# Optimization experiments

Measured on AMD Instinct MI355X. Metric: run time of the kernel, lower is better.

The kernel has to match this reference:

```python
import jax, jax.numpy as jnp
import numpy as np

NUM_LAYERS = 4
D_MODEL = 128
D_STATE = 16
DELTA_RANK = 8


def setup_inputs() -> dict:
    key = jax.random.key(0)
    ks = jax.random.split(key, 10)
    d, N, dr, L_ = D_MODEL, D_STATE, DELTA_RANK, NUM_LAYERS
    B, R, T = 4, 32, 1024
    x = jax.random.normal(ks[0], (B, R, T), dtype=jnp.float32)

    def w(k, shape, fan_in):
        return jax.random.normal(k, shape, dtype=jnp.float32) / np.sqrt(fan_in).astype(np.float32)

    inp_w = w(ks[1], (d, 1), 1)
    inp_b = jnp.zeros((d,), jnp.float32)
    outp_w = w(ks[2], (1, d), d)
    outp_b = jnp.zeros((1,), jnp.float32)
    ln_g = jnp.ones((L_, d), jnp.float32)
    ln_b = jnp.zeros((L_, d), jnp.float32)
    in_w = w(ks[3], (L_, 2 * d, d), d)
    conv_w = w(ks[4], (L_, d, 3), 3)
    conv_b = jnp.zeros((L_, d), jnp.float32)
    xp_w = w(ks[5], (L_, dr + 2 * N, d), d)
    dp_w = w(ks[6], (L_, d, dr), dr)
    # delta_proj bias = log(dt), dt ~ loguniform(dt_min, dt_max)
    dt = jnp.exp(jax.random.uniform(ks[7], (L_, d), dtype=jnp.float32) * (np.log(0.1) - np.log(0.001)) + np.log(0.001))
    dp_b = jnp.log(dt)
    # A_log = Re(log(-0.5 + i*imag)) = 0.5*log(0.25 + imag^2)
    A_imag = np.arange(1, N + 1, dtype=np.float32) / (1.0 + 2.0 * np.arange(N, dtype=np.float32))
    A_row = 0.5 * np.log(0.25 + A_imag ** 2)
    A_log = jnp.asarray(np.broadcast_to(A_row, (L_, d, N)).copy(), jnp.float32)
    Dp = 0.1 * jnp.ones((L_, d), jnp.float32)
    out_w = w(ks[8], (L_, d, d), d)
    return dict(x=x, inp_w=inp_w, inp_b=inp_b, outp_w=outp_w, outp_b=outp_b,
                ln_g=ln_g, ln_b=ln_b, in_w=in_w, conv_w=conv_w, conv_b=conv_b,
                xp_w=xp_w, dp_w=dp_w, dp_b=dp_b, A_log=A_log, Dp=Dp, out_w=out_w)


def _layernorm(x, g, b):
    mu = jnp.mean(x, -1, keepdims=True)
    v = jnp.var(x, -1, keepdims=True)
    return (x - mu) * jax.lax.rsqrt(v + 1e-5) * g + b


def _selective_scan(u, delta, A_log, Bm, Cm, Dp):
    # u, delta: (Bt, L, d); Bm, Cm: (Bt, L, N); A_log: (d, N); Dp: (d,)
    Bt, L, d = u.shape
    N = A_log.shape[1]
    A = -jnp.exp(A_log)  # (d, N)

    def step(x_prev, inp):
        u_t, dt_t, B_t, C_t = inp  # (Bt,d),(Bt,d),(Bt,N),(Bt,N)
        dA = jnp.exp(dt_t[..., None] * A)                       # (Bt,d,N)
        dBu = dt_t[..., None] * B_t[:, None, :] * u_t[..., None]  # (Bt,d,N)
        x_new = dA * x_prev + dBu
        y_t = jnp.einsum('bdn,bn->bd', x_new, C_t)
        return x_new, y_t

    x0 = jnp.zeros((Bt, d, N), dtype=u.dtype)
    _, ys = jax.lax.scan(step, x0, (u.swapaxes(0, 1), delta.swapaxes(0, 1),
                                    Bm.swapaxes(0, 1), Cm.swapaxes(0, 1)))
    return ys.swapaxes(0, 1) + u * Dp  # (Bt, L, d)


def _block(h, ln_g, ln_b, in_w, conv_w, conv_b, xp_w, dp_w, dp_b, A_log, Dp, out_w):
    Bt, L, d = h.shape
    dr = dp_w.shape[1]
    N = A_log.shape[1]
    z = _layernorm(h, ln_g, ln_b)
    xr = z @ in_w.T                      # (Bt, L, 2d)
    xi, res = jnp.split(xr, 2, axis=-1)
    # depthwise causal conv, kernel=3 (torch pad=2 then crop [:L] == left-pad 2)
    xp = jnp.pad(xi, ((0, 0), (2, 0), (0, 0)))
    xc = (xp[:, 0:L] * conv_w[:, 0] + xp[:, 1:L + 1] * conv_w[:, 1]
          + xp[:, 2:L + 2] * conv_w[:, 2]) + conv_b
    xc = jax.nn.silu(xc)
    dbc = xc @ xp_w.T                    # (Bt, L, dr + 2N)
    dlt, Bm, Cm = jnp.split(dbc, [dr, dr + N], axis=-1)
    delta = jax.nn.softplus(dlt @ dp_w.T + dp_b)  # (Bt, L, d)
    y = _selective_scan(xc, delta, A_log, Bm, Cm, Dp)
    y = y * jax.nn.silu(res)
    return y @ out_w.T


def reference(x, inp_w, inp_b, outp_w, outp_b, ln_g, ln_b, in_w, conv_w, conv_b,
              xp_w, dp_w, dp_b, A_log, Dp, out_w):
    B, R, T = x.shape
    h = x.reshape(B * R, T, 1) @ inp_w.T + inp_b  # (B*R, T, d)
    for i in range(ln_g.shape[0]):
        h = _block(h, ln_g[i], ln_b[i], in_w[i], conv_w[i], conv_b[i], xp_w[i],
                   dp_w[i], dp_b[i], A_log[i], Dp[i], out_w[i]) + h
    out = (h @ outp_w.T + outp_b)[..., 0]  # (B*R, T)
    return out.reshape(B, R, T)
```

## Files before the change

### kernel.cpp

```cpp
#include <hip/hip_runtime.h>
#include <math.h>

#define D 128
#define NSTATE 16
#define DR 8
#define T_SEQ 1024
#define NTOK 131072
#define SEG 8
#define SEGLEN 128
#define ZS 136
#define XRS2 132

typedef __attribute__((ext_vector_type(8))) short bf16x8;
typedef __attribute__((ext_vector_type(4))) float f32x4;

#define LOG2E 1.44269504088896340736f
#define LN2   0.69314718055994530942f

__device__ __forceinline__ float sigmoidf_(float x) {
    return __builtin_amdgcn_rcpf(1.0f + exp2f(-x * LOG2E));
}
__device__ __forceinline__ float softplusf_(float x) {
    float t = LN2 * __builtin_amdgcn_logf(1.0f + exp2f(x * LOG2E));
    return (x > 20.0f) ? x : t;
}
__device__ __forceinline__ short f2bf(float f) {
    union { float f; unsigned u; } v; v.f = f;
    unsigned r = v.u + 0x7FFFu + ((v.u >> 16) & 1u);
    return (short)(r >> 16);
}
__device__ __forceinline__ float bf2f(short s) {
    union { unsigned u; float f; } v; v.u = ((unsigned)(unsigned short)s) << 16;
    return v.f;
}


__global__ void k_prepw(const float* __restrict__ src, short* __restrict__ hi,
                        short* __restrict__ lo, int n) {
    int i = blockIdx.x * 256 + threadIdx.x;
    if (i < n) {
        float f = src[i];
        short hh = f2bf(f);
        hi[i] = hh;
        lo[i] = f2bf(f - bf2f(hh));
    }
}

__global__ void k_prepw_xp(const float* __restrict__ src, short* __restrict__ hi,
                           short* __restrict__ lo) {
    int i = blockIdx.x * 256 + threadIdx.x;
    if (i >= 4 * 48 * 128) return;
    int l = i / (48 * 128);
    int rem = i - l * 48 * 128;
    int j = rem >> 7, k = rem & 127;
    float f = (j < 40) ? src[(l * 40 + j) * 128 + k] : 0.f;
    short hh = f2bf(f);
    hi[i] = hh;
    lo[i] = f2bf(f - bf2f(hh));
}

__global__ void k_a2(const float* __restrict__ A_log, float* __restrict__ A2, int total) {
    int idx = blockIdx.x * blockDim.x + threadIdx.x;
    if (idx < total) A2[idx] = -__expf(A_log[idx]) * LOG2E;
}

__global__ void k_init_h(const float* __restrict__ x, const float* __restrict__ inp_w,
                         const float* __restrict__ inp_b, float* __restrict__ h) {
    int idx = blockIdx.x * blockDim.x + threadIdx.x;
    int tok = idx >> 7;
    int d = idx & 127;
    h[idx] = x[tok] * inp_w[d] + inp_b[d];
}

__global__ __launch_bounds__(256) void k_ln_inproj_conv(
    const float* __restrict__ h, const float* __restrict__ ln_g, const float* __restrict__ ln_b,
    const short* __restrict__ wh, const short* __restrict__ wl,
    const short* __restrict__ xph, const short* __restrict__ xpl,
    const float* __restrict__ conv_w, const float* __restrict__ conv_b,
    float* __restrict__ xc, float* __restrict__ res,
    float* __restrict__ bc, float* __restrict__ dlt)
{
    __shared__ __align__(16) short zsh[48 * ZS];
    __shared__ __align__(16) short zsl[48 * ZS];
    __shared__ __align__(16) float xr[34 * XRS2];
    __shared__ __align__(16) float dbc_l[32][52];
    const int tid = threadIdx.x;
    const int wv = tid >> 6, lane = tid & 63;
    const int tstart = blockIdx.x * 32;
    const int tin = tstart & (T_SEQ - 1);

    for (int r = wv; r < 34; r += 4) {
        int tr = tin + r - 2;
        if (tr < 0) {
            zsh[r * ZS + lane] = 0; zsh[r * ZS + lane + 64] = 0;
            zsl[r * ZS + lane] = 0; zsl[r * ZS + lane + 64] = 0;
            continue;
        }
        size_t row = (size_t)(tstart + r - 2) * D;
        float a = h[row + lane];
        float b = h[row + lane + 64];
        float s = a + b, ss = a * a + b * b;
        #pragma unroll
        for (int m = 1; m < 64; m <<= 1) { s += __shfl_xor(s, m); ss += __shfl_xor(ss, m); }
        float mu = s * (1.0f / 128.0f);
        float var = ss * (1.0f / 128.0f) - mu * mu;
        float rstd = rsqrtf(var + 1e-5f);
        float z0 = (a - mu) * rstd * ln_g[lane]      + ln_b[lane];
        float z1 = (b - mu) * rstd * ln_g[lane + 64] + ln_b[lane + 64];
        short h0 = f2bf(z0), h1 = f2bf(z1);
        zsh[r * ZS + lane]      = h0;
        zsh[r * ZS + lane + 64] = h1;
        zsl[r * ZS + lane]      = f2bf(z0 - bf2f(h0));
        zsl[r * ZS + lane + 64] = f2bf(z1 - bf2f(h1));
    }
    for (int i = tid; i < 14 * 128; i += 256) {
        int r = 34 + (i >> 7), c = i & 127;
        zsh[r * ZS + c] = 0;
        zsl[r * ZS + c] = 0;
    }

    const int colb = wv * 64 + (lane & 15);
    const int kb = (lane >> 4) * 8;
    bf16x8 bw[4][4];
    #pragma unroll
    for (int ct = 0; ct < 4; ++ct)
        #pragma unroll
        for (int kf = 0; kf < 4; ++kf)
            bw[ct][kf] = *(const bf16x8*)&wh[(colb + ct * 16) * 128 + kf * 32 + kb];
    __syncthreads();

    f32x4 acc[3][4];
    #pragma unroll
    for (int b = 0; b < 3; ++b)
        #pragma unroll
        for (int ct = 0; ct < 4; ++ct)
            acc[b][ct] = (f32x4){0.f, 0.f, 0.f, 0.f};

    #pragma unroll
    for (int b = 0; b < 3; ++b) {
        bf16x8 ah[4], al[4];
        const int rbase = (b * 16 + (lane & 15)) * ZS + kb;
        #pragma unroll
        for (int kf = 0; kf < 4; ++kf) {
            ah[kf] = *(const bf16x8*)&zsh[rbase + kf * 32];
            al[kf] = *(const bf16x8*)&zsl[rbase + kf * 32];
        }
        #pragma unroll
        for (int ct = 0; ct < 4; ++ct)
            #pragma unroll
            for (int kf = 0; kf < 4; ++kf) {
                acc[b][ct] = __builtin_amdgcn_mfma_f32_16x16x32_bf16(ah[kf], bw[ct][kf], acc[b][ct], 0, 0, 0);
                acc[b][ct] = __builtin_amdgcn_mfma_f32_16x16x32_bf16(al[kf], bw[ct][kf], acc[b][ct], 0, 0, 0);
            }
    }
    #pragma unroll
    for (int ct = 0; ct < 4; ++ct)
        #pragma unroll
        for (int kf = 0; kf < 4; ++kf)
            bw[ct][kf] = *(const bf16x8*)&wl[(colb + ct * 16) * 128 + kf * 32 + kb];
    #pragma unroll
    for (int b = 0; b < 3; ++b) {
        bf16x8 ah[4];
        const int rbase = (b * 16 + (lane & 15)) * ZS + kb;
        #pragma unroll
        for (int kf = 0; kf < 4; ++kf)
            ah[kf] = *(const bf16x8*)&zsh[rbase + kf * 32];
        #pragma unroll
        for (int ct = 0; ct < 4; ++ct)
            #pragma unroll
            for (int kf = 0; kf < 4; ++kf)
                acc[b][ct] = __builtin_amdgcn_mfma_f32_16x16x32_bf16(ah[kf], bw[ct][kf], acc[b][ct], 0, 0, 0);
    }

    if (wv < 2) {
        #pragma unroll
        for (int b = 0; b < 3; ++b)
            #pragma unroll
            for (int ct = 0; ct < 4; ++ct) {
                const int col = wv * 64 + ct * 16 + (lane & 15);
                #pragma unroll
                for (int i = 0; i < 4; ++i) {
                    int row = b * 16 + ((lane >> 4) << 2) + i;
                    if (row < 34) xr[row * XRS2 + col] = acc[b][ct][i];
                }
            }
    }
    __syncthreads();

    {
        int ch = tid & 127, s0 = (tid >> 7) * 16;
        float c0 = conv_w[ch * 3 + 0], c1 = conv_w[ch * 3 + 1], c2 = conv_w[ch * 3 + 2];
        float cb = conv_b[ch];
        float v0 = xr[(s0 + 0) * XRS2 + ch], v1 = xr[(s0 + 1) * XRS2 + ch];
        #pragma unroll
        for (int s = 0; s < 16; ++s) {
            float v2 = xr[(s0 + s + 2) * XRS2 + ch];
            float v = v0 * c0 + v1 * c1 + v2 * c2 + cb;
            v = v * sigmoidf_(v);
            xc[(size_t)(tstart + s0 + s) * D + ch] = v;
            short hh = f2bf(v);
            zsh[(s0 + s) * ZS + ch] = hh;
            zsl[(s0 + s) * ZS + ch] = f2bf(v - bf2f(hh));
            v0 = v1; v1 = v2;
        }
    }
    __syncthreads();

    if (wv >= 2) {
        #pragma unroll
        for (int b = 0; b < 3; ++b)
            #pragma unroll
            for (int ct = 0; ct < 4; ++ct) {
                const int col = (wv - 2) * 64 + ct * 16 + (lane & 15);
                #pragma unroll
                for (int i = 0; i < 4; ++i) {
                    int row = b * 16 + ((lane >> 4) << 2) + i;
                    if (row >= 2 && row < 34) xr[row * XRS2 + col] = acc[b][ct][i];
                }
            }
    }
    for (int tile = wv; tile < 6; tile += 4) {
        const int b = tile & 1, ct = tile >> 1;
        const int jcol = ct * 16 + (lane & 15);
        const int rbase = (b * 16 + (lane & 15)) * ZS + kb;
        bf16x8 ah[4], al[4], bh[4];
        #pragma unroll
        for (int kf = 0; kf < 4; ++kf) {
            ah[kf] = *(const bf16x8*)&zsh[rbase + kf * 32];
            al[kf] = *(const bf16x8*)&zsl[rbase + kf * 32];
            bh[kf] = *(const bf16x8*)&xph[jcol * 128 + kf * 32 + kb];
        }
        f32x4 a2 = (f32x4){0.f, 0.f, 0.f, 0.f};
        #pragma unroll
        for (int kf = 0; kf < 4; ++kf) {
            a2 = __builtin_amdgcn_mfma_f32_16x16x32_bf16(ah[kf], bh[kf], a2, 0, 0, 0);
            a2 = __builtin_amdgcn_mfma_f32_16x16x32_bf16(al[kf], bh[kf], a2, 0, 0, 0);
        }
        #pragma unroll
        for (int kf = 0; kf < 4; ++kf) {
            bh[kf] = *(const bf16x8*)&xpl[jcol * 128 + kf * 32 + kb];
            a2 = __builtin_amdgcn_mfma_f32_16x16x32_bf16(ah[kf], bh[kf], a2, 0, 0, 0);
        }
        #pragma unroll
        for (int i = 0; i < 4; ++i) {
            int t = b * 16 + ((lane >> 4) << 2) + i;
            dbc_l[t][jcol] = a2[i];
        }
    }
    __syncthreads();

    for (int fi = tid; fi < 1024; fi += 256) {
        int r = fi >> 5, c4 = fi & 31;
        *(float4*)&res[(size_t)(tstart + r) * D + c4 * 4] =
            *(const float4*)&xr[(r + 2) * XRS2 + c4 * 4];
    }
    {
        int t = tid >> 3, q = tid & 7;
        *(float4*)&bc[(size_t)(tstart + t) * 32 + q * 4] = *(const float4*)&dbc_l[t][8 + q * 4];
    }
    if (tid < 64) {
        int t = tid >> 1, j4 = tid & 1;
        *(float4*)&dlt[(size_t)(tstart + t) * 8 + j4 * 4] = *(const float4*)&dbc_l[t][j4 * 4];
    }
}

__global__ __launch_bounds__(256) void k_scan1(
    const float* __restrict__ xc, const float* __restrict__ bc,
    const float* __restrict__ dlt,
    const float* __restrict__ dp_w, const float* __restrict__ dp_b,
    const float* __restrict__ A2,
    float* __restrict__ Pbuf, float* __restrict__ Fbuf)
{
    const int tid = threadIdx.x;
    const int d = tid & 127;
    const int segid = blockIdx.x * 2 + (tid >> 7);
    const size_t segbase = (size_t)segid * SEGLEN;

    float dpw[DR];
    #pragma unroll
    for (int r = 0; r < DR; ++r) dpw[r] = dp_w[d * DR + r];
    const float dpb = dp_b[d];
    float A2r[NSTATE];
    #pragma unroll
    for (int n = 0; n < NSTATE; ++n) A2r[n] = A2[d * NSTATE + n];
    float xs[NSTATE];
    #pragma unroll
    for (int n = 0; n < NSTATE; ++n) xs[n] = 0.f;
    float S = 0.f;

    float4 dl0 = *(const float4*)&dlt[segbase * 8];
    float4 dl1 = *(const float4*)&dlt[segbase * 8 + 4];
    float4 B0 = *(const float4*)&bc[segbase * 32 + 0];
    float4 B1 = *(const float4*)&bc[segbase * 32 + 4];
    float4 B2 = *(const float4*)&bc[segbase * 32 + 8];
    float4 B3 = *(const float4*)&bc[segbase * 32 + 12];
    float uv = xc[segbase * D + d];

    for (int tl = 0; tl < SEGLEN; ++tl) {
        float4 cd0 = dl0, cd1 = dl1, cB0 = B0, cB1 = B1, cB2 = B2, cB3 = B3;
        float cu = uv;
        if (tl + 1 < SEGLEN) {
            const size_t nt = segbase + tl + 1;
            dl0 = *(const float4*)&dlt[nt * 8];
            dl1 = *(const float4*)&dlt[nt * 8 + 4];
            B0 = *(const float4*)&bc[nt * 32 + 0];
            B1 = *(const float4*)&bc[nt * 32 + 4];
            B2 = *(const float4*)&bc[nt * 32 + 8];
            B3 = *(const float4*)&bc[nt * 32 + 12];
            uv = xc[nt * D + d];
        }
        float v = dpb;
        v = fmaf(cd0.x, dpw[0], v); v = fmaf(cd0.y, dpw[1], v);
        v = fmaf(cd0.z, dpw[2], v); v = fmaf(cd0.w, dpw[3], v);
        v = fmaf(cd1.x, dpw[4], v); v = fmaf(cd1.y, dpw[5], v);
        v = fmaf(cd1.z, dpw[6], v); v = fmaf(cd1.w, dpw[7], v);
        float dt = softplusf_(v);
        float duv = dt * cu;
        S += dt;
        xs[0]  = fmaf(exp2f(dt * A2r[0]),  xs[0],  duv * cB0.x);
        xs[1]  = fmaf(exp2f(dt * A2r[1]),  xs[1],  duv * cB0.y);
        xs[2]  = fmaf(exp2f(dt * A2r[2]),  xs[2],  duv * cB0.z);
        xs[3]  = fmaf(exp2f(dt * A2r[3]),  xs[3],  duv * cB0.w);
        xs[4]  = fmaf(exp2f(dt * A2r[4]),  xs[4],  duv * cB1.x);
        xs[5]  = fmaf(exp2f(dt * A2r[5]),  xs[5],  duv * cB1.y);
        xs[6]  = fmaf(exp2f(dt * A2r[6]),  xs[6],  duv * cB1.z);
        xs[7]  = fmaf(exp2f(dt * A2r[7]),  xs[7],  duv * cB1.w);
        xs[8]  = fmaf(exp2f(dt * A2r[8]),  xs[8],  duv * cB2.x);
        xs[9]  = fmaf(exp2f(dt * A2r[9]),  xs[9],  duv * cB2.y);
        xs[10] = fmaf(exp2f(dt * A2r[10]), xs[10], duv * cB2.z);
        xs[11] = fmaf(exp2f(dt * A2r[11]), xs[11], duv * cB2.w);
        xs[12] = fmaf(exp2f(dt * A2r[12]), xs[12], duv * cB3.x);
        xs[13] = fmaf(exp2f(dt * A2r[13]), xs[13], duv * cB3.y);
        xs[14] = fmaf(exp2f(dt * A2r[14]), xs[14], duv * cB3.z);
        xs[15] = fmaf(exp2f(dt * A2r[15]), xs[15], duv * cB3.w);
    }
    const size_t o = ((size_t)segid * D + d) * NSTATE;
    #pragma unroll
    for (int nq = 0; nq < 4; ++nq) {
        *(float4*)&Fbuf[o + nq * 4] =
            make_float4(xs[nq*4], xs[nq*4+1], xs[nq*4+2], xs[nq*4+3]);
        *(float4*)&Pbuf[o + nq * 4] =
            make_float4(exp2f(A2r[nq*4] * S), exp2f(A2r[nq*4+1] * S),
                        exp2f(A2r[nq*4+2] * S), exp2f(A2r[nq*4+3] * S));
    }
}

__global__ __launch_bounds__(256) void k_scan2(
    const float* __restrict__ xc, const float* __restrict__ bc,
    const float* __restrict__ dlt,
    const float* __restrict__ dp_w, const float* __restrict__ dp_b,
    const float* __restrict__ A2, const float* __restrict__ Dp,
    const float* __restrict__ Pbuf, const float* __restrict__ Fbuf,
    float* __restrict__ resy)
{
    const int tid = threadIdx.x;
    const int d = tid & 127;
    const int segid = blockIdx.x * 2 + (tid >> 7);
    const int bt = segid >> 3, seg = segid & 7;
    const size_t segbase = (size_t)segid * SEGLEN;

    float dpw[DR];
    #pragma unroll
    for (int r = 0; r < DR; ++r) dpw[r] = dp_w[d * DR + r];
    const float dpb = dp_b[d];
    float A2r[NSTATE];
    #pragma unroll
    for (int n = 0; n < NSTATE; ++n) A2r[n] = A2[d * NSTATE + n];
    const float Dpd = Dp[d];

    float xs[NSTATE];
    #pragma unroll
    for (int n = 0; n < NSTATE; ++n) xs[n] = 0.f;
    for (int s = 0; s < seg; ++s) {
        const size_t idx = ((size_t)(bt * SEG + s) * D + d) * NSTATE;
        #pragma unroll
        for (int nq = 0; nq < 4; ++nq) {
            float4 P = *(const float4*)&Pbuf[idx + nq * 4];
            float4 F = *(const float4*)&Fbuf[idx + nq * 4];
            xs[nq*4+0] = fmaf(P.x, xs[nq*4+0], F.x);
            xs[nq*4+1] = fmaf(P.y, xs[nq*4+1], F.y);
            xs[nq*4+2] = fmaf(P.z, xs[nq*4+2], F.z);
            xs[nq*4+3] = fmaf(P.w, xs[nq*4+3], F.w);
        }
    }

    float4 dl0 = *(const float4*)&dlt[segbase * 8];
    float4 dl1 = *(const float4*)&dlt[segbase * 8 + 4];
    float4 B0 = *(const float4*)&bc[segbase * 32 + 0];
    float4 B1 = *(const float4*)&bc[segbase * 32 + 4];
    float4 B2 = *(const float4*)&bc[segbase * 32 + 8];
    float4 B3 = *(const float4*)&bc[segbase * 32 + 12];
    float4 C0 = *(const float4*)&bc[segbase * 32 + 16];
    float4 C1 = *(const float4*)&bc[segbase * 32 + 20];
    float4 C2 = *(const float4*)&bc[segbase * 32 + 24];
    float4 C3 = *(const float4*)&bc[segbase * 32 + 28];
    float uv = xc[segbase * D + d];
    float rg = resy[segbase * D + d];

    for (int tl = 0; tl < SEGLEN; ++tl) {
        float4 cd0 = dl0, cd1 = dl1;
        float4 cB0 = B0, cB1 = B1, cB2 = B2, cB3 = B3;
        float4 cC0 = C0, cC1 = C1, cC2 = C2, cC3 = C3;
        float cu = uv, cg = rg;
        if (tl + 1 < SEGLEN) {
            const size_t nt = segbase + tl + 1;
            dl0 = *(const float4*)&dlt[nt * 8];
            dl1 = *(const float4*)&dlt[nt * 8 + 4];
            B0 = *(const float4*)&bc[nt * 32 + 0];
            B1 = *(const float4*)&bc[nt * 32 + 4];
            B2 = *(const float4*)&bc[nt * 32 + 8];
            B3 = *(const float4*)&bc[nt * 32 + 12];
            C0 = *(const float4*)&bc[nt * 32 + 16];
            C1 = *(const float4*)&bc[nt * 32 + 20];
            C2 = *(const float4*)&bc[nt * 32 + 24];
            C3 = *(const float4*)&bc[nt * 32 + 28];
            uv = xc[nt * D + d];
            rg = resy[nt * D + d];
        }
        float v = dpb;
        v = fmaf(cd0.x, dpw[0], v); v = fmaf(cd0.y, dpw[1], v);
        v = fmaf(cd0.z, dpw[2], v); v = fmaf(cd0.w, dpw[3], v);
        v = fmaf(cd1.x, dpw[4], v); v = fmaf(cd1.y, dpw[5], v);
        v = fmaf(cd1.z, dpw[6], v); v = fmaf(cd1.w, dpw[7], v);
        float dt = softplusf_(v);
        float duv = dt * cu;
        xs[0]  = fmaf(exp2f(dt * A2r[0]),  xs[0],  duv * cB0.x);
        xs[1]  = fmaf(exp2f(dt * A2r[1]),  xs[1],  duv * cB0.y);
        xs[2]  = fmaf(exp2f(dt * A2r[2]),  xs[2],  duv * cB0.z);
        xs[3]  = fmaf(exp2f(dt * A2r[3]),  xs[3],  duv * cB0.w);
        xs[4]  = fmaf(exp2f(dt * A2r[4]),  xs[4],  duv * cB1.x);
        xs[5]  = fmaf(exp2f(dt * A2r[5]),  xs[5],  duv * cB1.y);
        xs[6]  = fmaf(exp2f(dt * A2r[6]),  xs[6],  duv * cB1.z);
        xs[7]  = fmaf(exp2f(dt * A2r[7]),  xs[7],  duv * cB1.w);
        xs[8]  = fmaf(exp2f(dt * A2r[8]),  xs[8],  duv * cB2.x);
        xs[9]  = fmaf(exp2f(dt * A2r[9]),  xs[9],  duv * cB2.y);
        xs[10] = fmaf(exp2f(dt * A2r[10]), xs[10], duv * cB2.z);
        xs[11] = fmaf(exp2f(dt * A2r[11]), xs[11], duv * cB2.w);
        xs[12] = fmaf(exp2f(dt * A2r[12]), xs[12], duv * cB3.x);
        xs[13] = fmaf(exp2f(dt * A2r[13]), xs[13], duv * cB3.y);
        xs[14] = fmaf(exp2f(dt * A2r[14]), xs[14], duv * cB3.z);
        xs[15] = fmaf(exp2f(dt * A2r[15]), xs[15], duv * cB3.w);
        float y = xs[0] * cC0.x;
        y = fmaf(xs[1],  cC0.y, y);
        y = fmaf(xs[2],  cC0.z, y);
        y = fmaf(xs[3],  cC0.w, y);
        y = fmaf(xs[4],  cC1.x, y);
        y = fmaf(xs[5],  cC1.y, y);
        y = fmaf(xs[6],  cC1.z, y);
        y = fmaf(xs[7],  cC1.w, y);
        y = fmaf(xs[8],  cC2.x, y);
        y = fmaf(xs[9],  cC2.y, y);
        y = fmaf(xs[10], cC2.z, y);
        y = fmaf(xs[11], cC2.w, y);
        y = fmaf(xs[12], cC3.x, y);
        y = fmaf(xs[13], cC3.y, y);
        y = fmaf(xs[14], cC3.z, y);
        y = fmaf(xs[15], cC3.w, y);
        y = fmaf(cu, Dpd, y);
        resy[(segbase + tl) * D + d] = y * (cg * sigmoidf_(cg));
    }
}

__global__ __launch_bounds__(256) void k_outproj(
    const float* __restrict__ y, const short* __restrict__ wh, const short* __restrict__ wl,
    float* __restrict__ h)
{
    __shared__ __align__(16) short ysh[32 * ZS];
    __shared__ __align__(16) short ysl[32 * ZS];
    const int tid = threadIdx.x;
    const int wv = tid >> 6, lane = tid & 63;
    const size_t tb = (size_t)blockIdx.x * 32;

    #pragma unroll
    for (int i = 0; i < 4; ++i) {
        int idx = tid + i * 256;
        int row = idx >> 5, c4 = idx & 31;
        float4 v = *(const float4*)&y[(tb + row) * D + c4 * 4];
        short h0 = f2bf(v.x), h1 = f2bf(v.y), h2 = f2bf(v.z), h3 = f2bf(v.w);
        *(short4*)&ysh[row * ZS + c4 * 4] = make_short4(h0, h1, h2, h3);
        *(short4*)&ysl[row * ZS + c4 * 4] = make_short4(
            f2bf(v.x - bf2f(h0)), f2bf(v.y - bf2f(h1)),
            f2bf(v.z - bf2f(h2)), f2bf(v.w - bf2f(h3)));
    }

    const int colb = wv * 32 + (lane & 15);
    const int kb = (lane >> 4) * 8;
    bf16x8 bw[2][4];
    #pragma unroll
    for (int ct = 0; ct < 2; ++ct)
        #pragma unroll
        for (int kf = 0; kf < 4; ++kf)
            bw[ct][kf] = *(const bf16x8*)&wh[(colb + ct * 16) * 128 + kf * 32 + kb];
    __syncthreads();

    f32x4 acc[2][2];
    #pragma unroll
    for (int b = 0; b < 2; ++b)
        #pragma unroll
        for (int ct = 0; ct < 2; ++ct)
            acc[b][ct] = (f32x4){0.f, 0.f, 0.f, 0.f};

    #pragma unroll
    for (int b = 0; b < 2; ++b) {
        bf16x8 ah[4], al[4];
        const int rbase = (b * 16 + (lane & 15)) * ZS + kb;
        #pragma unroll
        for (int kf = 0; kf < 4; ++kf) {
            ah[kf] = *(const bf16x8*)&ysh[rbase + kf * 32];
            al[kf] = *(const bf16x8*)&ysl[rbase + kf * 32];
        }
        #pragma unroll
        for (int ct = 0; ct < 2; ++ct)
            #pragma unroll
            for (int kf = 0; kf < 4; ++kf) {
                acc[b][ct] = __builtin_amdgcn_mfma_f32_16x16x32_bf16(ah[kf], bw[ct][kf], acc[b][ct], 0, 0, 0);
                acc[b][ct] = __builtin_amdgcn_mfma_f32_16x16x32_bf16(al[kf], bw[ct][kf], acc[b][ct], 0, 0, 0);
            }
    }
    #pragma unroll
    for (int ct = 0; ct < 2; ++ct)
        #pragma unroll
        for (int kf = 0; kf < 4; ++kf)
            bw[ct][kf] = *(const bf16x8*)&wl[(colb + ct * 16) * 128 + kf * 32 + kb];
    #pragma unroll
    for (int b = 0; b < 2; ++b) {
        bf16x8 ah[4];
        const int rbase = (b * 16 + (lane & 15)) * ZS + kb;
        #pragma unroll
        for (int kf = 0; kf < 4; ++kf)
            ah[kf] = *(const bf16x8*)&ysh[rbase + kf * 32];
        #pragma unroll
        for (int ct = 0; ct < 2; ++ct)
            #pragma unroll
            for (int kf = 0; kf < 4; ++kf)
                acc[b][ct] = __builtin_amdgcn_mfma_f32_16x16x32_bf16(ah[kf], bw[ct][kf], acc[b][ct], 0, 0, 0);
    }

    #pragma unroll
    for (int b = 0; b < 2; ++b)
        #pragma unroll
        for (int ct = 0; ct < 2; ++ct) {
            const int col = wv * 32 + ct * 16 + (lane & 15);
            #pragma unroll
            for (int i = 0; i < 4; ++i) {
                int row = b * 16 + ((lane >> 4) << 2) + i;
                size_t o = (tb + row) * D + col;
                h[o] += acc[b][ct][i];
            }
        }
}

__global__ __launch_bounds__(256) void k_final(
    const float* __restrict__ h, const float* __restrict__ outp_w,
    const float* __restrict__ outp_b, float* __restrict__ out)
{
    const int tid = threadIdx.x;
    const int lane = tid & 63;
    const size_t tok = (size_t)blockIdx.x * 4 + (tid >> 6);
    float a = h[tok * D + lane] * outp_w[lane] + h[tok * D + lane + 64] * outp_w[lane + 64];
    #pragma unroll
    for (int m = 1; m < 64; m <<= 1) a += __shfl_xor(a, m);
    if (lane == 0) out[tok] = a + outp_b[0];
}

extern "C" void kernel_launch(void* const* d_in, const int* in_sizes, int n_in,
                              void* d_out, int out_size, void* d_ws, size_t ws_size,
                              hipStream_t stream)
{
    const float* x      = (const float*)d_in[0];
    const float* inp_w  = (const float*)d_in[1];
    const float* inp_b  = (const float*)d_in[2];
    const float* outp_w = (const float*)d_in[3];
    const float* outp_b = (const float*)d_in[4];
    const float* ln_g   = (const float*)d_in[5];
    const float* ln_b   = (const float*)d_in[6];
    const float* in_w   = (const float*)d_in[7];
    const float* conv_w = (const float*)d_in[8];
    const float* conv_b = (const float*)d_in[9];
    const float* xp_w   = (const float*)d_in[10];
    const float* dp_w   = (const float*)d_in[11];
    const float* dp_b   = (const float*)d_in[12];
    const float* A_log  = (const float*)d_in[13];
    const float* Dp     = (const float*)d_in[14];
    const float* out_w  = (const float*)d_in[15];

    float* ws = (float*)d_ws;
    size_t off = 0;
    float* h      = ws + off; off += (size_t)NTOK * D;
    float* xc     = ws + off; off += (size_t)NTOK * D;
    float* resy   = ws + off; off += (size_t)NTOK * D;
    float* bc     = ws + off; off += (size_t)NTOK * 32;
    float* dlt    = ws + off; off += (size_t)NTOK * 8;
    float* Pbuf   = ws + off; off += 128 * SEG * 2048;
    float* Fbuf   = ws + off; off += 128 * SEG * 2048;
    short* in_wBh = (short*)(ws + off); off += 4 * 256 * 128 / 2;
    short* in_wBl = (short*)(ws + off); off += 4 * 256 * 128 / 2;
    short* out_wBh= (short*)(ws + off); off += 4 * 128 * 128 / 2;
    short* out_wBl= (short*)(ws + off); off += 4 * 128 * 128 / 2;
    short* xp_wBh = (short*)(ws + off); off += 4 * 48 * 128 / 2;
    short* xp_wBl = (short*)(ws + off); off += 4 * 48 * 128 / 2;
    float* A2     = ws + off; off += 4 * 128 * 16;
    if (ws_size < off * sizeof(float)) return;

    k_prepw<<<(4 * 256 * 128 + 255) / 256, 256, 0, stream>>>(in_w, in_wBh, in_wBl, 4 * 256 * 128);
    k_prepw<<<(4 * 128 * 128 + 255) / 256, 256, 0, stream>>>(out_w, out_wBh, out_wBl, 4 * 128 * 128);
    k_prepw_xp<<<(4 * 48 * 128 + 255) / 256, 256, 0, stream>>>(xp_w, xp_wBh, xp_wBl);
    k_a2<<<(4 * 128 * 16 + 255) / 256, 256, 0, stream>>>(A_log, A2, 4 * 128 * 16);
    k_init_h<<<NTOK * D / 256, 256, 0, stream>>>(x, inp_w, inp_b, h);

    for (int l = 0; l < 4; ++l) {
        k_ln_inproj_conv<<<NTOK / 32, 256, 0, stream>>>(
            h, ln_g + l * 128, ln_b + l * 128,
            in_wBh + l * 256 * 128, in_wBl + l * 256 * 128,
            xp_wBh + l * 48 * 128, xp_wBl + l * 48 * 128,
            conv_w + l * 128 * 3, conv_b + l * 128, xc, resy, bc, dlt);
        k_scan1<<<512, 256, 0, stream>>>(xc, bc, dlt, dp_w + l * 128 * 8, dp_b + l * 128,
                                         A2 + l * 128 * 16, Pbuf, Fbuf);
        k_scan2<<<512, 256, 0, stream>>>(xc, bc, dlt, dp_w + l * 128 * 8, dp_b + l * 128,
                                         A2 + l * 128 * 16, Dp + l * 128, Pbuf, Fbuf, resy);
        k_outproj<<<NTOK / 32, 256, 0, stream>>>(resy, out_wBh + l * 128 * 128,
                                                 out_wBl + l * 128 * 128, h);
    }
    k_final<<<NTOK / 4, 256, 0, stream>>>(h, outp_w, outp_b, (float*)d_out);
}
```

Before: 1.639 ms.

## Double scan segments and store per-segment delta sums instead of decay products

The chunked selective scan now uses 16 segments of 64 steps instead of 8 of 128, which doubles the scan grids and shortens each thread's serial recurrence. The first pass stores only the scalar delta sum per segment and channel, and the second pass recomputes the decay factors with exp2 when it combines earlier segments. This cuts the P buffer traffic but adds exp2 work and a longer serial prefix (up to 15 segments) in the second pass. The per-state F loads also change from float4 to scalar loads.

```diff
diff --git a/kernel.cpp b/kernel.cpp
--- a/kernel.cpp
+++ b/kernel.cpp
@@ -6,8 +6,8 @@
 #define DR 8
 #define T_SEQ 1024
 #define NTOK 131072
-#define SEG 8
-#define SEGLEN 128
+#define SEG 16
+#define SEGLEN 64
 #define ZS 136
 #define XRS2 132
 
@@ -269,7 +269,7 @@
     const float* __restrict__ dlt,
     const float* __restrict__ dp_w, const float* __restrict__ dp_b,
     const float* __restrict__ A2,
-    float* __restrict__ Pbuf, float* __restrict__ Fbuf)
+    float* __restrict__ Sbuf, float* __restrict__ Fbuf)
 {
     const int tid = threadIdx.x;
     const int d = tid & 127;
@@ -336,13 +336,10 @@
     }
     const size_t o = ((size_t)segid * D + d) * NSTATE;
     #pragma unroll
-    for (int nq = 0; nq < 4; ++nq) {
+    for (int nq = 0; nq < 4; ++nq)
         *(float4*)&Fbuf[o + nq * 4] =
             make_float4(xs[nq*4], xs[nq*4+1], xs[nq*4+2], xs[nq*4+3]);
-        *(float4*)&Pbuf[o + nq * 4] =
-            make_float4(exp2f(A2r[nq*4] * S), exp2f(A2r[nq*4+1] * S),
-                        exp2f(A2r[nq*4+2] * S), exp2f(A2r[nq*4+3] * S));
-    }
+    Sbuf[(size_t)segid * D + d] = S;
 }
 
 __global__ __launch_bounds__(256) void k_scan2(
@@ -350,13 +347,14 @@
     const float* __restrict__ dlt,
     const float* __restrict__ dp_w, const float* __restrict__ dp_b,
     const float* __restrict__ A2, const float* __restrict__ Dp,
-    const float* __restrict__ Pbuf, const float* __restrict__ Fbuf,
+    const float* __restrict__ Sbuf, const float* __restrict__ Fbuf,
     float* __restrict__ resy)
 {
     const int tid = threadIdx.x;
     const int d = tid & 127;
     const int segid = blockIdx.x * 2 + (tid >> 7);
-    const int bt = segid >> 3, seg = segid & 7;
+    const int seg = segid & (SEG - 1);
+    const int seg0 = segid - seg;
     const size_t segbase = (size_t)segid * SEGLEN;
 
     float dpw[DR];
@@ -372,15 +370,13 @@
     #pragma unroll
     for (int n = 0; n < NSTATE; ++n) xs[n] = 0.f;
     for (int s = 0; s < seg; ++s) {
-        const size_t idx = ((size_t)(bt * SEG + s) * D + d) * NSTATE;
-        #pragma unroll
-        for (int nq = 0; nq < 4; ++nq) {
-            float4 P = *(const float4*)&Pbuf[idx + nq * 4];
-            float4 F = *(const float4*)&Fbuf[idx + nq * 4];
-            xs[nq*4+0] = fmaf(P.x, xs[nq*4+0], F.x);
-            xs[nq*4+1] = fmaf(P.y, xs[nq*4+1], F.y);
-            xs[nq*4+2] = fmaf(P.z, xs[nq*4+2], F.z);
-            xs[nq*4+3] = fmaf(P.w, xs[nq*4+3], F.w);
+        const int sid = seg0 + s;
+        const float Sv = Sbuf[(size_t)sid * D + d];
+        const size_t idx = ((size_t)sid * D + d) * NSTATE;
+        #pragma unroll
+        for (int n = 0; n < NSTATE; ++n) {
+            float F = Fbuf[idx + n];
+            xs[n] = fmaf(exp2f(A2r[n] * Sv), xs[n], F);
         }
     }
 
@@ -591,8 +587,8 @@
     float* resy   = ws + off; off += (size_t)NTOK * D;
     float* bc     = ws + off; off += (size_t)NTOK * 32;
     float* dlt    = ws + off; off += (size_t)NTOK * 8;
-    float* Pbuf   = ws + off; off += 128 * SEG * 2048;
     float* Fbuf   = ws + off; off += 128 * SEG * 2048;
+    float* Sbuf   = ws + off; off += 128 * SEG * 128;
     short* in_wBh = (short*)(ws + off); off += 4 * 256 * 128 / 2;
     short* in_wBl = (short*)(ws + off); off += 4 * 256 * 128 / 2;
     short* out_wBh= (short*)(ws + off); off += 4 * 128 * 128 / 2;
@@ -614,10 +610,10 @@
             in_wBh + l * 256 * 128, in_wBl + l * 256 * 128,
             xp_wBh + l * 48 * 128, xp_wBl + l * 48 * 128,
             conv_w + l * 128 * 3, conv_b + l * 128, xc, resy, bc, dlt);
-        k_scan1<<<512, 256, 0, stream>>>(xc, bc, dlt, dp_w + l * 128 * 8, dp_b + l * 128,
-                                         A2 + l * 128 * 16, Pbuf, Fbuf);
-        k_scan2<<<512, 256, 0, stream>>>(xc, bc, dlt, dp_w + l * 128 * 8, dp_b + l * 128,
-                                         A2 + l * 128 * 16, Dp + l * 128, Pbuf, Fbuf, resy);
+        k_scan1<<<1024, 256, 0, stream>>>(xc, bc, dlt, dp_w + l * 128 * 8, dp_b + l * 128,
+                                          A2 + l * 128 * 16, Sbuf, Fbuf);
+        k_scan2<<<1024, 256, 0, stream>>>(xc, bc, dlt, dp_w + l * 128 * 8, dp_b + l * 128,
+                                          A2 + l * 128 * 16, Dp + l * 128, Sbuf, Fbuf, resy);
         k_outproj<<<NTOK / 32, 256, 0, stream>>>(resy, out_wBh + l * 128 * 128,
                                                  out_wBl + l * 128 * 128, h);
     }
```

After: 1.584 ms. 1.03x faster.
